# Performance work log

Measured on AMD Instinct MI355X. Metric: run time of the kernel, lower is better.

Reference implementation:

```python
import jax, jax.numpy as jnp
import numpy as np

DIM = 1024
NUM_HEADS = 16
HEAD_DIM = DIM // NUM_HEADS
SCALE = HEAD_DIM ** -0.5


def setup_inputs() -> dict:
    key = jax.random.key(0)
    ks = jax.random.split(key, 12)
    B, N, M, C = 4, 512, 2048, DIM
    x = jax.random.normal(ks[0], (B, N, C), dtype=jnp.float32)
    context = jax.random.normal(ks[1], (B, M, C), dtype=jnp.float32)
    mask = jax.random.randint(ks[2], (B, M), 0, 2, dtype=jnp.int32)
    mask = mask.at[:, 0].set(1)  # ensure at least one valid key per row
    w = 0.02
    Wq = jax.random.normal(ks[3], (C, C), dtype=jnp.float32) * w
    bq = jnp.zeros((C,), dtype=jnp.float32)
    Wk = jax.random.normal(ks[4], (C, C), dtype=jnp.float32) * w
    bk = jnp.zeros((C,), dtype=jnp.float32)
    Wv = jax.random.normal(ks[5], (C, C), dtype=jnp.float32) * w
    bv = jnp.zeros((C,), dtype=jnp.float32)
    Wo = jax.random.normal(ks[6], (C, C), dtype=jnp.float32) * w
    bo = jnp.zeros((C,), dtype=jnp.float32)
    return {"x": x, "context": context, "ctx_key_padding_mask": mask,
            "Wq": Wq, "bq": bq, "Wk": Wk, "bk": bk,
            "Wv": Wv, "bv": bv, "Wo": Wo, "bo": bo}


def reference(x, context, ctx_key_padding_mask, Wq, bq, Wk, bk, Wv, bv, Wo, bo):
    B, N, C = x.shape
    M = context.shape[1]
    H, D = NUM_HEADS, HEAD_DIM
    # torch nn.Linear: y = x @ W.T + b
    q = (x @ Wq.T + bq).reshape(B, N, H, D)
    k = (context @ Wk.T + bk).reshape(B, M, H, D)
    v = (context @ Wv.T + bv).reshape(B, M, H, D)
    scores = jnp.einsum('bnhd,bmhd->bhnm', q, k) * SCALE  # [B,H,N,M]
    neg = jnp.finfo(scores.dtype).min
    bias = jnp.where(ctx_key_padding_mask[:, None, None, :] != 0, 0.0, neg).astype(scores.dtype)
    attn = jax.nn.softmax(scores + bias, axis=-1)
    out = jnp.einsum('bhnm,bmhd->bnhd', attn, v).reshape(B, N, C)
    return out @ Wo.T + bo
```

## Files before the change

kernel.cpp:

```cpp
#include <hip/hip_runtime.h>
#include <hip/hip_bf16.h>
#include <stdint.h>


typedef __attribute__((ext_vector_type(4))) float f32x4;
typedef __attribute__((ext_vector_type(8))) __bf16 bf16x8;
typedef __attribute__((ext_vector_type(8))) unsigned short u16x8;

#define DEVI __device__ __forceinline__

#define QSC (0.125f * 1.44269504088896f)

DEVI f32x4 mfma16(u16x8 a, u16x8 b, f32x4 c) {
  return __builtin_amdgcn_mfma_f32_16x16x32_bf16(
      __builtin_bit_cast(bf16x8, a), __builtin_bit_cast(bf16x8, b), c, 0, 0, 0);
}

DEVI unsigned short f2bf(float f) {
  union { float f; unsigned int u; } x; x.f = f;
  unsigned int u = x.u;
  return (unsigned short)((u + 0x7fffu + ((u >> 16) & 1u)) >> 16);
}

DEVI float exp2_fast(float x) {
#if __has_builtin(__builtin_amdgcn_exp2f)
  return __builtin_amdgcn_exp2f(x);
#else
  return exp2f(x);
#endif
}

DEVI void llds16(const void* g, void* l) {
  __builtin_amdgcn_global_load_lds(
      (const __attribute__((address_space(1))) void*)g,
      (__attribute__((address_space(3))) void*)l, 16, 0, 0);
}

__global__ __launch_bounds__(256)
void compact_mask(const int* __restrict__ mask, int* __restrict__ cnt,
                  int* __restrict__ idx) {
  __shared__ int psum[256];
  const int b = blockIdx.x, tid = threadIdx.x;
  const int* mb = mask + b * 2048;
  int v[8], s = 0;
#pragma unroll
  for (int j = 0; j < 8; ++j) { v[j] = (mb[tid * 8 + j] != 0); s += v[j]; }
  psum[tid] = s;
  __syncthreads();
  for (int off = 1; off < 256; off <<= 1) {
    int t = (tid >= off) ? psum[tid - off] : 0;
    __syncthreads();
    psum[tid] += t;
    __syncthreads();
  }
  int base = tid ? psum[tid - 1] : 0;
#pragma unroll
  for (int j = 0; j < 8; ++j)
    if (v[j]) { idx[b * 2048 + base] = tid * 8 + j; ++base; }
  if (tid == 255) cnt[b] = psum[255];
}

__global__ __launch_bounds__(256)
void cast_fused(const float* __restrict__ x, const float* __restrict__ ctx,
                const float* __restrict__ wq, const float* __restrict__ wk,
                const float* __restrict__ wv, const float* __restrict__ wo,
                const int* __restrict__ cnt, const int* __restrict__ idx,
                unsigned short* __restrict__ xb, unsigned short* __restrict__ cb,
                unsigned short* __restrict__ wqb, unsigned short* __restrict__ wkb,
                unsigned short* __restrict__ wvb, unsigned short* __restrict__ wob) {
  int bid = blockIdx.x;
  const int tid = threadIdx.x;
  if (bid >= 2048 && bid < 10240) {
    int r = bid - 2048;
    int b = r >> 11, j = r & 2047;
    int c = cnt[b];
    unsigned short* dst = cb + (size_t)r * 1024 + tid * 4;
    if (j >= c) {
      if (j < ((c + 255) & ~255)) {
        ushort4 z; z.x = z.y = z.z = z.w = 0;
        *(ushort4*)dst = z;
      }
      return;
    }
    const float* src = ctx + ((size_t)(b * 2048 + idx[b * 2048 + j])) * 1024 + tid * 4;
    const float4 v = *(const float4*)src;
    ushort4 o;
    o.x = f2bf(v.x); o.y = f2bf(v.y); o.z = f2bf(v.z); o.w = f2bf(v.w);
    *(ushort4*)dst = o;
    return;
  }
  const float* src; unsigned short* dst; float scale = 1.f;
  if (bid < 2048)        { src = x;   dst = xb; }
  else if (bid < 11264)  { src = wq;  dst = wqb; bid -= 10240; scale = QSC; }
  else if (bid < 12288)  { src = wk;  dst = wkb; bid -= 11264; }
  else if (bid < 13312)  { src = wv;  dst = wvb; bid -= 12288; }
  else                   { src = wo;  dst = wob; bid -= 13312; }
  int e = (bid * 256 + tid) * 4;
  const float4 v = *(const float4*)(src + e);
  ushort4 o;
  o.x = f2bf(v.x * scale); o.y = f2bf(v.y * scale);
  o.z = f2bf(v.z * scale); o.w = f2bf(v.w * scale);
  *(ushort4*)(dst + e) = o;
}

DEVI void epi_store(f32x4 (&acc)[4][4], const float* __restrict__ bias,
                    float bscale, void* __restrict__ Cout,
                    int bm, int bn, int logS, int mode,
                    unsigned short* cst, int tid, int wave, int l15, int quad) {
  const int wm = wave & 1, wn = wave >> 1;
  __syncthreads();
  for (int half = 0; half < 2; ++half) {
    if (wm == half) {
#pragma unroll
      for (int mi = 0; mi < 4; ++mi)
#pragma unroll
        for (int ni = 0; ni < 4; ++ni)
#pragma unroll
          for (int r = 0; r < 4; ++r) {
            int lrow = mi * 16 + quad * 4 + r;
            int lcol = wn * 64 + ni * 16 + l15;
            unsigned short bv = f2bf(acc[mi][ni][r] + bias[bn + lcol] * bscale);
            if (mode == 0) cst[lrow * 136 + lcol] = bv;
            else           cst[lcol * 72 + lrow] = bv;
          }
    }
    __syncthreads();
    if (mode == 0) {
      int lrow = tid >> 2, cc = (tid & 3) * 32;
      int row = bm + half * 64 + lrow;
      int S = 1 << logS;
      int b = row >> logS, sl = row & (S - 1);
#pragma unroll
      for (int j = 0; j < 4; ++j) {
        int col = bn + cc + j * 8;
        int h = col >> 6, d8 = (col & 63) >> 3;
        size_t base = (((size_t)(b * 16 + h)) << logS) * 64 +
                      (size_t)(sl >> 4) * 1024 + d8 * 128 + (sl & 15) * 8;
        *(u16x8*)&((unsigned short*)Cout)[base] =
            *(const u16x8*)&cst[lrow * 136 + cc + j * 8];
      }
    } else {
      int c = tid >> 1, rc = (tid & 1) * 32;
      int gc = bn + c, h = gc >> 6, d = gc & 63;
      int b = bm >> 11;
#pragma unroll
      for (int j = 0; j < 4; ++j) {
        int key = (bm & 2047) + half * 64 + rc + j * 8;
        size_t base = (size_t)(b * 16 + h) * 131072 +
                      (size_t)(((key >> 6) * 4 + (d >> 4)) * 8 + ((key >> 3) & 7)) * 128 +
                      (d & 15) * 8;
        *(u16x8*)&((unsigned short*)Cout)[base] =
            *(const u16x8*)&cst[c * 72 + rc + j * 8];
      }
    }
    __syncthreads();
  }
}

DEVI void kv_body(const unsigned short* __restrict__ A,
                  const unsigned short* __restrict__ WK,
                  const unsigned short* __restrict__ WV,
                  const float* __restrict__ bk, const float* __restrict__ bv,
                  unsigned short* __restrict__ kh, unsigned short* __restrict__ vt,
                  int bm, int bn, unsigned short* sh) {
  constexpr int K = 1024;
  unsigned short* As = sh;
  unsigned short* Ks = sh + 128 * 64;
  unsigned short* Vs = sh + 2 * 128 * 64;

  const int tid = threadIdx.x;
  const int wave = tid >> 6, lane = tid & 63;
  const int l15 = lane & 15, quad = lane >> 4;
  const int wm = wave & 1, wn = wave >> 1;

  f32x4 ak[4][4] = {}, av[4][4] = {};

  for (int k0 = 0; k0 < K; k0 += 64) {
    __syncthreads();
#pragma unroll
    for (int c = 0; c < 4; ++c) {
      int s = c * 256 + tid;
      int m = s >> 3;
      int k8 = (s & 7) ^ (m & 7);
      llds16(A + (size_t)(bm + m) * K + k0 + k8 * 8, &As[s * 8]);
      llds16(WK + (size_t)(bn + m) * K + k0 + k8 * 8, &Ks[s * 8]);
      llds16(WV + (size_t)(bn + m) * K + k0 + k8 * 8, &Vs[s * 8]);
    }
    __syncthreads();
#pragma unroll
    for (int ks = 0; ks < 2; ++ks) {
      const int k8 = ks * 4 + quad;
      u16x8 af[4], bf[4];
#pragma unroll
      for (int i = 0; i < 4; ++i) {
        int m = wm * 64 + i * 16 + l15;
        af[i] = *(const u16x8*)(&As[(m * 8 + (k8 ^ (m & 7))) * 8]);
      }
#pragma unroll
      for (int i = 0; i < 4; ++i) {
        int n = wn * 64 + i * 16 + l15;
        bf[i] = *(const u16x8*)(&Ks[(n * 8 + (k8 ^ (n & 7))) * 8]);
      }
#pragma unroll
      for (int mi = 0; mi < 4; ++mi)
#pragma unroll
        for (int ni = 0; ni < 4; ++ni)
          ak[mi][ni] = mfma16(af[mi], bf[ni], ak[mi][ni]);
#pragma unroll
      for (int i = 0; i < 4; ++i) {
        int n = wn * 64 + i * 16 + l15;
        bf[i] = *(const u16x8*)(&Vs[(n * 8 + (k8 ^ (n & 7))) * 8]);
      }
#pragma unroll
      for (int mi = 0; mi < 4; ++mi)
#pragma unroll
        for (int ni = 0; ni < 4; ++ni)
          av[mi][ni] = mfma16(af[mi], bf[ni], av[mi][ni]);
    }
  }

  epi_store(ak, bk, 1.f, kh, bm, bn, 11, 0, sh, tid, wave, l15, quad);
  epi_store(av, bv, 1.f, vt, bm, bn, 11, 2, sh, tid, wave, l15, quad);
}

DEVI void q_body(const unsigned short* __restrict__ A,
                 const unsigned short* __restrict__ W,
                 const float* __restrict__ bias,
                 unsigned short* __restrict__ Cout,
                 int bm, int bn, unsigned short* sh) {
  constexpr int K = 1024;
  unsigned short* As = sh;
  unsigned short* Bs = sh + 128 * 64;

  const int tid = threadIdx.x;
  const int wave = tid >> 6, lane = tid & 63;
  const int l15 = lane & 15, quad = lane >> 4;
  const int wm = wave & 1, wn = wave >> 1;

  f32x4 acc[4][4] = {};

  for (int k0 = 0; k0 < K; k0 += 64) {
    __syncthreads();
#pragma unroll
    for (int c = 0; c < 4; ++c) {
      int s = c * 256 + tid;
      int m = s >> 3;
      int k8 = (s & 7) ^ (m & 7);
      llds16(A + (size_t)(bm + m) * K + k0 + k8 * 8, &As[s * 8]);
      llds16(W + (size_t)(bn + m) * K + k0 + k8 * 8, &Bs[s * 8]);
    }
    __syncthreads();
#pragma unroll
    for (int ks = 0; ks < 2; ++ks) {
      const int k8 = ks * 4 + quad;
      u16x8 af[4], bf[4];
#pragma unroll
      for (int i = 0; i < 4; ++i) {
        int m = wm * 64 + i * 16 + l15;
        af[i] = *(const u16x8*)(&As[(m * 8 + (k8 ^ (m & 7))) * 8]);
        int n = wn * 64 + i * 16 + l15;
        bf[i] = *(const u16x8*)(&Bs[(n * 8 + (k8 ^ (n & 7))) * 8]);
      }
#pragma unroll
      for (int mi = 0; mi < 4; ++mi)
#pragma unroll
        for (int ni = 0; ni < 4; ++ni)
          acc[mi][ni] = mfma16(af[mi], bf[ni], acc[mi][ni]);
    }
  }

  epi_store(acc, bias, QSC, Cout, bm, bn, 9, 0, sh, tid, wave, l15, quad);
}

__global__ __launch_bounds__(256, 2)
void gemm_qkv(const unsigned short* __restrict__ xb,
              const unsigned short* __restrict__ cb,
              const unsigned short* __restrict__ wq,
              const unsigned short* __restrict__ wk,
              const unsigned short* __restrict__ wv,
              const float* __restrict__ bq, const float* __restrict__ bk,
              const float* __restrict__ bv,
              const int* __restrict__ cnt,
              unsigned short* __restrict__ qh, unsigned short* __restrict__ kh,
              unsigned short* __restrict__ vt) {
  __shared__ __align__(16) unsigned short sh[128 * 64 * 3];
  const int x = blockIdx.x, y = blockIdx.y;
  if (y < 8) {
    const int bm = x * 128;
    const int cpad = (cnt[bm >> 11] + 255) & ~255;
    if ((bm & 2047) >= cpad) return;
    kv_body(cb, wk, wv, bk, bv, kh, vt, bm, y * 128, sh);
  } else {
    q_body(xb, wq, bq, qh, (x & 15) * 128, (y - 8) * 512 + (x >> 4) * 128, sh);
  }
}

__global__ __launch_bounds__(256)
void gemm_o(const unsigned short* __restrict__ A,
            const unsigned short* __restrict__ W,
            const float* __restrict__ bo, float* __restrict__ out) {
  constexpr int K = 1024;
  __shared__ __align__(16) unsigned short As[64 * 64];
  __shared__ __align__(16) unsigned short Bs[128 * 64];

  const int tid = threadIdx.x;
  const int wave = tid >> 6, lane = tid & 63;
  const int l15 = lane & 15, quad = lane >> 4;
  const int bm = blockIdx.x * 64, bn = blockIdx.y * 128;

  f32x4 acc[4][2] = {};

  for (int k0 = 0; k0 < K; k0 += 64) {
    __syncthreads();
#pragma unroll
    for (int c = 0; c < 2; ++c) {
      int s = c * 256 + tid;
      int m = s >> 3, k8 = (s & 7) ^ (m & 7);
      llds16(A + (size_t)(bm + m) * K + k0 + k8 * 8, &As[s * 8]);
    }
#pragma unroll
    for (int c = 0; c < 4; ++c) {
      int s = c * 256 + tid;
      int m = s >> 3, k8 = (s & 7) ^ (m & 7);
      llds16(W + (size_t)(bn + m) * K + k0 + k8 * 8, &Bs[s * 8]);
    }
    __syncthreads();
#pragma unroll
    for (int ks = 0; ks < 2; ++ks) {
      const int k8 = ks * 4 + quad;
      u16x8 af[4], bf[2];
#pragma unroll
      for (int i = 0; i < 4; ++i) {
        int m = i * 16 + l15;
        af[i] = *(const u16x8*)(&As[(m * 8 + (k8 ^ (m & 7))) * 8]);
      }
#pragma unroll
      for (int i = 0; i < 2; ++i) {
        int n = wave * 32 + i * 16 + l15;
        bf[i] = *(const u16x8*)(&Bs[(n * 8 + (k8 ^ (n & 7))) * 8]);
      }
#pragma unroll
      for (int mi = 0; mi < 4; ++mi)
#pragma unroll
        for (int ni = 0; ni < 2; ++ni)
          acc[mi][ni] = mfma16(af[mi], bf[ni], acc[mi][ni]);
    }
  }

#pragma unroll
  for (int mi = 0; mi < 4; ++mi)
#pragma unroll
    for (int ni = 0; ni < 2; ++ni)
#pragma unroll
      for (int r = 0; r < 4; ++r) {
        int row = bm + mi * 16 + quad * 4 + r;
        int col = bn + wave * 32 + ni * 16 + l15;
        out[(size_t)row * 1024 + col] = acc[mi][ni][r] + bo[col];
      }
}

#define PS 72
__global__ __launch_bounds__(256, 1)
void attn_kernel(const unsigned short* __restrict__ Q,
                 const unsigned short* __restrict__ K,
                 const unsigned short* __restrict__ Vt,
                 const int* __restrict__ cnt,
                 unsigned short* __restrict__ O) {
  __shared__ float bias_lds[2048];
  __shared__ __align__(16) unsigned short p_lds[4][2][16 * PS];
  __shared__ float l_lds[4][64];
  __shared__ __align__(16) float o_comb[64][68];

  const int tid = threadIdx.x;
  const int wave = tid >> 6, lane = tid & 63;
  const int l15 = lane & 15, quad = lane >> 4;
  const int bh = blockIdx.x, b = bh >> 4, h = bh & 15;
  const int q0 = blockIdx.y * 64;

  const int c = cnt[b];
  const int T = (c + 255) >> 8;

  for (int i = tid; i < 2048; i += 256)
    bias_lds[i] = (i < c) ? -8.f : -1e30f;
  __syncthreads();

  const unsigned short* Qb = Q + (size_t)bh * 32768 + (size_t)(q0 >> 4) * 1024;
  const unsigned short* Kb = K + (size_t)bh * 131072;
  const unsigned short* Vb = Vt + (size_t)bh * 131072;

  u16x8 aq[4][2];
#pragma unroll
  for (int qg = 0; qg < 4; ++qg)
#pragma unroll
    for (int ks = 0; ks < 2; ++ks)
      aq[qg][ks] = *(const u16x8*)(Qb + ((qg * 8 + ks * 4 + quad) * 16 + l15) * 8);

  f32x4 o_acc[4][4] = {};
  float l_s[4] = {0.f, 0.f, 0.f, 0.f};

  u16x8 kf[2][4];

  auto load_k = [&](int kb) {
    const int kg0 = kb >> 4;
#pragma unroll
    for (int ns = 0; ns < 4; ++ns)
#pragma unroll
      for (int ks = 0; ks < 2; ++ks)
        kf[ks][ns] = *(const u16x8*)(Kb + (((size_t)(kg0 + ns) * 8 + ks * 4 + quad) * 16 + l15) * 8);
  };

  load_k(wave * 64);

#pragma unroll 1
  for (int t = 0; t < T; ++t) {
    const int kb = wave * 64 + t * 256;
    const int kb_next = kb + (t + 1 < T ? 256 : 0);

    u16x8 vf[2][4];
    const int kt4 = (kb >> 6) * 4;
#pragma unroll
    for (int nd = 0; nd < 4; ++nd)
#pragma unroll
      for (int ks = 0; ks < 2; ++ks)
        vf[ks][nd] = *(const u16x8*)(Vb + (((size_t)(kt4 + nd) * 8 + ks * 4 + quad) * 16 + l15) * 8);
    f32x4 bfr[4];
#pragma unroll
    for (int ns = 0; ns < 4; ++ns)
      bfr[ns] = *(const f32x4*)&bias_lds[kb + ns * 16 + quad * 4];

#pragma unroll
    for (int qg = 0; qg < 4; ++qg) {
      f32x4 sfr[4];
#pragma unroll
      for (int ns = 0; ns < 4; ++ns) {
        f32x4 sa = bfr[ns];
#pragma unroll
        for (int ks = 0; ks < 2; ++ks)
          sa = mfma16(kf[ks][ns], aq[qg][ks], sa);
        sfr[ns] = sa;
      }

      if (qg == 3) load_k(kb_next);

      float rsum = 0.f;
#pragma unroll
      for (int ns = 0; ns < 4; ++ns) {
        unsigned int pr[4];
#pragma unroll
        for (int r = 0; r < 4; ++r) {
          float p = exp2_fast(sfr[ns][r]);
          unsigned int u = __builtin_bit_cast(unsigned int, p) & 0xffff0000u;
          rsum += __builtin_bit_cast(float, u);
          pr[r] = u;
        }
        uint2 pw;
        pw.x = __builtin_amdgcn_perm(pr[1], pr[0], 0x07060302u);
        pw.y = __builtin_amdgcn_perm(pr[3], pr[2], 0x07060302u);
        *(uint2*)&p_lds[wave][qg & 1][l15 * PS + ns * 16 + quad * 4] = pw;
      }
      rsum += __shfl_xor(rsum, 16, 64);
      rsum += __shfl_xor(rsum, 32, 64);
      l_s[qg] += rsum;

#pragma unroll
      for (int ks = 0; ks < 2; ++ks) {
        u16x8 pf = *(const u16x8*)&p_lds[wave][qg & 1][l15 * PS + ks * 32 + quad * 8];
#pragma unroll
        for (int nd = 0; nd < 4; ++nd)
          o_acc[qg][nd] = mfma16(pf, vf[ks][nd], o_acc[qg][nd]);
      }
    }
  }

  if (quad == 0) {
#pragma unroll
    for (int qg = 0; qg < 4; ++qg)
      l_lds[wave][qg * 16 + l15] = l_s[qg];
  }
  __syncthreads();

  for (int w = 0; w < 4; ++w) {
    if (wave == w) {
#pragma unroll
      for (int qg = 0; qg < 4; ++qg)
#pragma unroll
        for (int r = 0; r < 4; ++r) {
          const int q = qg * 16 + quad * 4 + r;
#pragma unroll
          for (int nd = 0; nd < 4; ++nd) {
            const int d = nd * 16 + l15;
            float v = o_acc[qg][nd][r];
            if (w == 0) o_comb[q][d] = v;
            else        o_comb[q][d] += v;
          }
        }
    }
    __syncthreads();
  }

  {
    const int q = tid >> 2, dc = (tid & 3) * 16;
    const float inv = 1.f / (l_lds[0][q] + l_lds[1][q] + l_lds[2][q] + l_lds[3][q]);
    unsigned short* Ob = O + ((size_t)(b * 512 + q0 + q)) * 1024 + h * 64 + dc;
    u16x8 o1, o2;
#pragma unroll
    for (int j = 0; j < 8; ++j) o1[j] = f2bf(o_comb[q][dc + j] * inv);
#pragma unroll
    for (int j = 0; j < 8; ++j) o2[j] = f2bf(o_comb[q][dc + 8 + j] * inv);
    *(u16x8*)(Ob) = o1;
    *(u16x8*)(Ob + 8) = o2;
  }
}

extern "C" void kernel_launch(void* const* d_in, const int* in_sizes, int n_in,
                              void* d_out, int out_size, void* d_ws, size_t ws_size,
                              hipStream_t stream) {
  const float* x   = (const float*)d_in[0];
  const float* ctx = (const float*)d_in[1];
  const int* mask  = (const int*)d_in[2];
  const float* Wq  = (const float*)d_in[3];
  const float* bq  = (const float*)d_in[4];
  const float* Wk  = (const float*)d_in[5];
  const float* bk  = (const float*)d_in[6];
  const float* Wv  = (const float*)d_in[7];
  const float* bv  = (const float*)d_in[8];
  const float* Wo  = (const float*)d_in[9];
  const float* bo  = (const float*)d_in[10];

  char* ws = (char*)d_ws;
  unsigned short* xb  = (unsigned short*)(ws + ((size_t)0  << 20));
  unsigned short* cb  = (unsigned short*)(ws + ((size_t)4  << 20));
  unsigned short* wqb = (unsigned short*)(ws + ((size_t)20 << 20));
  unsigned short* wkb = (unsigned short*)(ws + ((size_t)22 << 20));
  unsigned short* wvb = (unsigned short*)(ws + ((size_t)24 << 20));
  unsigned short* wob = (unsigned short*)(ws + ((size_t)26 << 20));
  unsigned short* qh  = (unsigned short*)(ws + ((size_t)28 << 20));
  unsigned short* kh  = (unsigned short*)(ws + ((size_t)32 << 20));
  unsigned short* vt  = (unsigned short*)(ws + ((size_t)48 << 20));
  unsigned short* ah  = (unsigned short*)(ws + ((size_t)64 << 20));
  int* cnt = (int*)d_out;
  int* idx = (int*)d_out + 4;

  compact_mask<<<4, 256, 0, stream>>>(mask, cnt, idx);
  cast_fused<<<14336, 256, 0, stream>>>(x, ctx, Wq, Wk, Wv, Wo, cnt, idx,
                                        xb, cb, wqb, wkb, wvb, wob);
  gemm_qkv<<<dim3(64, 10), 256, 0, stream>>>(xb, cb, wqb, wkb, wvb,
                                             bq, bk, bv, cnt, qh, kh, vt);
  attn_kernel<<<dim3(64, 8), 256, 0, stream>>>(qh, kh, vt, cnt, ah);
  gemm_o<<<dim3(32, 8), 256, 0, stream>>>(ah, wob, bo, (float*)d_out);
}
```

Baseline: 204.5 us.

## Compact QKV grid to valid key blocks and drop attention bias LDS

The QKV projection now uses a flattened 1D grid. Block ids map onto only the valid (mask-compacted) key row blocks per batch, followed by the query blocks, so skipped blocks no longer exit early and the schedule is dense. The attention kernel drops the 8KB bias LDS array and its init barrier and computes the mask bias in registers, taking a fast constant path for fully valid tiles. This lowers LDS use so two blocks can fit per CU (launch_bounds 256,2). The mask count buffers move from the output to workspace; the risk is register pressure under the tighter occupancy bound.

New measurement: 192.4 us. 1.06x faster.

```diff
diff --git a/kernel.cpp b/kernel.cpp
--- a/kernel.cpp
+++ b/kernel.cpp
@@ -284,14 +284,19 @@
               unsigned short* __restrict__ qh, unsigned short* __restrict__ kh,
               unsigned short* __restrict__ vt) {
   __shared__ __align__(16) unsigned short sh[128 * 64 * 3];
-  const int x = blockIdx.x, y = blockIdx.y;
-  if (y < 8) {
-    const int bm = x * 128;
-    const int cpad = (cnt[bm >> 11] + 255) & ~255;
-    if ((bm & 2047) >= cpad) return;
-    kv_body(cb, wk, wv, bk, bv, kh, vt, bm, y * 128, sh);
-  } else {
-    q_body(xb, wq, bq, qh, (x & 15) * 128, (y - 8) * 512 + (x >> 4) * 128, sh);
+  const int id = blockIdx.x;
+  const int nb0 = ((cnt[0] + 255) & ~255) >> 7, nb1 = ((cnt[1] + 255) & ~255) >> 7;
+  const int nb2 = ((cnt[2] + 255) & ~255) >> 7, nb3 = ((cnt[3] + 255) & ~255) >> 7;
+  const int L = nb0 + nb1 + nb2 + nb3;
+  if (id < L * 8) {
+    int xl = id >> 3, y = id & 7, b = 0;
+    if (xl >= nb0) { xl -= nb0; b = 1;
+      if (xl >= nb1) { xl -= nb1; b = 2;
+        if (xl >= nb2) { xl -= nb2; b = 3; } } }
+    kv_body(cb, wk, wv, bk, bv, kh, vt, b * 2048 + xl * 128, y * 128, sh);
+  } else if (id < L * 8 + 128) {
+    const int q = id - L * 8;
+    q_body(xb, wq, bq, qh, (q & 15) * 128, (q >> 4) * 128, sh);
   }
 }
 
@@ -360,13 +365,12 @@
 }
 
 #define PS 72
-__global__ __launch_bounds__(256, 1)
+__global__ __launch_bounds__(256, 2)
 void attn_kernel(const unsigned short* __restrict__ Q,
                  const unsigned short* __restrict__ K,
                  const unsigned short* __restrict__ Vt,
                  const int* __restrict__ cnt,
                  unsigned short* __restrict__ O) {
-  __shared__ float bias_lds[2048];
   __shared__ __align__(16) unsigned short p_lds[4][2][16 * PS];
   __shared__ float l_lds[4][64];
   __shared__ __align__(16) float o_comb[64][68];
@@ -380,10 +384,6 @@
   const int c = cnt[b];
   const int T = (c + 255) >> 8;
 
-  for (int i = tid; i < 2048; i += 256)
-    bias_lds[i] = (i < c) ? -8.f : -1e30f;
-  __syncthreads();
-
   const unsigned short* Qb = Q + (size_t)bh * 32768 + (size_t)(q0 >> 4) * 1024;
   const unsigned short* Kb = K + (size_t)bh * 131072;
   const unsigned short* Vb = Vt + (size_t)bh * 131072;
@@ -423,10 +423,19 @@
 #pragma unroll
       for (int ks = 0; ks < 2; ++ks)
         vf[ks][nd] = *(const u16x8*)(Vb + (((size_t)(kt4 + nd) * 8 + ks * 4 + quad) * 16 + l15) * 8);
+
     f32x4 bfr[4];
-#pragma unroll
-    for (int ns = 0; ns < 4; ++ns)
-      bfr[ns] = *(const f32x4*)&bias_lds[kb + ns * 16 + quad * 4];
+    if (kb + 64 <= c) {
+#pragma unroll
+      for (int ns = 0; ns < 4; ++ns)
+        bfr[ns] = f32x4{-8.f, -8.f, -8.f, -8.f};
+    } else {
+#pragma unroll
+      for (int ns = 0; ns < 4; ++ns)
+#pragma unroll
+        for (int r = 0; r < 4; ++r)
+          bfr[ns][r] = (kb + ns * 16 + quad * 4 + r < c) ? -8.f : -1e30f;
+    }
 
 #pragma unroll
     for (int qg = 0; qg < 4; ++qg) {
@@ -538,14 +547,14 @@
   unsigned short* kh  = (unsigned short*)(ws + ((size_t)32 << 20));
   unsigned short* vt  = (unsigned short*)(ws + ((size_t)48 << 20));
   unsigned short* ah  = (unsigned short*)(ws + ((size_t)64 << 20));
-  int* cnt = (int*)d_out;
-  int* idx = (int*)d_out + 4;
+  int* cnt = (int*)(ws + ((size_t)72 << 20));
+  int* idx = cnt + 4;
 
   compact_mask<<<4, 256, 0, stream>>>(mask, cnt, idx);
   cast_fused<<<14336, 256, 0, stream>>>(x, ctx, Wq, Wk, Wv, Wo, cnt, idx,
                                         xb, cb, wqb, wkb, wvb, wob);
-  gemm_qkv<<<dim3(64, 10), 256, 0, stream>>>(xb, cb, wqb, wkb, wvb,
-                                             bq, bk, bv, cnt, qh, kh, vt);
+  gemm_qkv<<<640, 256, 0, stream>>>(xb, cb, wqb, wkb, wvb,
+                                    bq, bk, bv, cnt, qh, kh, vt);
   attn_kernel<<<dim3(64, 8), 256, 0, stream>>>(qh, kh, vt, cnt, ah);
   gemm_o<<<dim3(32, 8), 256, 0, stream>>>(ah, wob, bo, (float*)d_out);
 }
```
